# Kernel optimization log

Hardware: AMD Instinct MI355X
Metric: run time of the kernel (lower is better)

The kernel has to match this reference:

```python
import jax, jax.numpy as jnp
import numpy as np

N = 50000; E = 600000; D = 128; NB = 20; L = 3; H = 64; NG = 512; ZMAX = 100
CUTOFF = 5.0

def setup_inputs() -> dict:
    key = jax.random.key(0)
    ks = jax.random.split(key, 32)
    inp = {}
    inp['at_no'] = jax.random.randint(ks[0], (N,), 0, ZMAX)
    inp['pos'] = jax.random.normal(ks[1], (N, 3), dtype=jnp.float32) * 3.0
    inp['edge_index'] = jax.random.randint(ks[2], (2, E), 0, N)
    inp['batch'] = jnp.sort(jax.random.randint(ks[3], (N,), 0, NG))
    def w(k, shape, fan_in):
        return (jax.random.normal(k, shape, dtype=jnp.float32) / np.sqrt(fan_in)).astype(jnp.float32)
    inp['emb'] = w(ks[4], (ZMAX, D), 1.0)
    # per-block filter net: rbf -> 3D
    inp['Wf'] = w(ks[5], (L, NB, 3 * D), NB); inp['bf'] = jnp.zeros((L, 3 * D), jnp.float32)
    # per-block message scalar MLP: D -> D -> 3D
    inp['Wm1'] = w(ks[6], (L, D, D), D);      inp['bm1'] = jnp.zeros((L, D), jnp.float32)
    inp['Wm2'] = w(ks[7], (L, D, 3 * D), D);  inp['bm2'] = jnp.zeros((L, 3 * D), jnp.float32)
    # per-block update: U, V channel-mixing on vectors; MLP 2D -> D -> 3D
    inp['U'] = w(ks[8], (L, D, D), D)
    inp['V'] = w(ks[9], (L, D, D), D)
    inp['Wu1'] = w(ks[10], (L, 2 * D, D), 2 * D); inp['bu1'] = jnp.zeros((L, D), jnp.float32)
    inp['Wu2'] = w(ks[11], (L, D, 3 * D), D);     inp['bu2'] = jnp.zeros((L, 3 * D), jnp.float32)
    # scalar output head: D -> H -> 1, graph sum
    inp['Wo1'] = w(ks[12], (D, H), D); inp['bo1'] = jnp.zeros((H,), jnp.float32)
    inp['Wo2'] = w(ks[13], (H, 1), H); inp['bo2'] = jnp.zeros((1,), jnp.float32)
    return inp

def _painn(at_no, pos, edge_index, batch, emb, Wf, bf, Wm1, bm1, Wm2, bm2,
           U, V, Wu1, bu1, Wu2, bu2, Wo1, bo1, Wo2, bo2):
    src, dst = edge_index[0], edge_index[1]
    vec = pos[dst] - pos[src]                       # [E,3]
    dist = jnp.sqrt(jnp.sum(vec * vec, axis=-1, keepdims=True) + 1e-12)  # [E,1]
    dirv = vec / dist                               # [E,3] (rsh l=1)
    n = jnp.arange(1, NB + 1, dtype=jnp.float32)
    rbf = jnp.sin(n * jnp.pi * dist / CUTOFF) / dist            # [E,NB] Bessel
    fcut = 0.5 * (jnp.cos(jnp.pi * dist / CUTOFF) + 1.0) * (dist < CUTOFF)  # [E,1]

    x = emb[at_no]                                  # [N,D]
    v = jnp.zeros((x.shape[0], 3, D), x.dtype)      # [N,3,D]

    for l in range(L):
        # ---- message ----
        filt = (rbf @ Wf[l] + bf[l]) * fcut                     # [E,3D]
        phi = jax.nn.silu(x @ Wm1[l] + bm1[l]) @ Wm2[l] + bm2[l]  # [N,3D]
        m = phi[src] * filt                                     # [E,3D]
        ds, dv1, dv2 = m[:, :D], m[:, D:2 * D], m[:, 2 * D:]
        dv = dv1[:, None, :] * dirv[:, :, None] + dv2[:, None, :] * v[src]  # [E,3,D]
        x = x + jax.ops.segment_sum(ds, dst, num_segments=N)
        v = v + jax.ops.segment_sum(dv, dst, num_segments=N)
        # ---- update ----
        Uv = jnp.einsum('ncd,de->nce', v, U[l])
        Vv = jnp.einsum('ncd,de->nce', v, V[l])
        Vn = jnp.sqrt(jnp.sum(Vv * Vv, axis=1) + 1e-8)          # [N,D]
        a = jax.nn.silu(jnp.concatenate([x, Vn], axis=-1) @ Wu1[l] + bu1[l]) @ Wu2[l] + bu2[l]
        avv, asv, ass = a[:, :D], a[:, D:2 * D], a[:, 2 * D:]
        x = x + ass + asv * jnp.sum(Uv * Vv, axis=1)
        v = v + avv[:, None, :] * Uv

    node_out = jax.nn.silu(x @ Wo1 + bo1) @ Wo2 + bo2           # [N,1]
    return jax.ops.segment_sum(node_out, batch, num_segments=NG)  # [NG,1]

def reference(at_no, pos, edge_index, batch, emb, Wf, bf, Wm1, bm1, Wm2, bm2,
              U, V, Wu1, bu1, Wu2, bu2, Wo1, bo1, Wo2, bo2):
    return _painn(at_no, pos, edge_index, batch, emb, Wf, bf, Wm1, bm1, Wm2, bm2,
                  U, V, Wu1, bu1, Wu2, bu2, Wo1, bo1, Wo2, bo2)
```

## Files before the change

### kernel.cpp

```cpp
#include <hip/hip_runtime.h>
#include <math.h>

#define NN 50000
#define NE 600000
#define ECAP 230000
#define DD 128
#define D3 384
#define NB_ 20
#define HH 64
#define NG_ 512
#define LSZ 180224

typedef short v8s __attribute__((ext_vector_type(8)));
typedef short v4sh __attribute__((ext_vector_type(4)));
typedef float v4f __attribute__((ext_vector_type(4)));

__device__ __forceinline__ float silu_f(float z) { return z / (1.0f + expf(-z)); }

__device__ __forceinline__ short f2bf(float f) {
  unsigned u = __float_as_uint(f);
  u += 0x7FFF + ((u >> 16) & 1);
  return (short)(u >> 16);
}
__device__ __forceinline__ float bf2f(short s) {
  return __uint_as_float(((unsigned)(unsigned short)s) << 16);
}
__device__ __forceinline__ void split2(float x, short& h, short& l) {
  h = f2bf(x);
  l = f2bf(x - bf2f(h));
}
#define SPLIT8(f0, f1, ah, al) { short h,l; \
  split2(f0.x,h,l); ah[0]=h; al[0]=l;  split2(f0.y,h,l); ah[1]=h; al[1]=l; \
  split2(f0.z,h,l); ah[2]=h; al[2]=l;  split2(f0.w,h,l); ah[3]=h; al[3]=l; \
  split2(f1.x,h,l); ah[4]=h; al[4]=l;  split2(f1.y,h,l); ah[5]=h; al[5]=l; \
  split2(f1.z,h,l); ah[6]=h; al[6]=l;  split2(f1.w,h,l); ah[7]=h; al[7]=l; }
__device__ __forceinline__ void split_store4(float4 f, short* hp, short* lp) {
  short h0,l0,h1,l1,h2,l2,h3,l3;
  split2(f.x,h0,l0); split2(f.y,h1,l1); split2(f.z,h2,l2); split2(f.w,h3,l3);
  v4sh hv = {h0,h1,h2,h3}, lv = {l0,l1,l2,l3};
  *(v4sh*)hp = hv; *(v4sh*)lp = lv;
}
#define MFMA3(acc, ah, al, bh, bl) \
  acc = __builtin_amdgcn_mfma_f32_16x16x32_bf16(ah, bh, acc, 0, 0, 0); \
  acc = __builtin_amdgcn_mfma_f32_16x16x32_bf16(al, bh, acc, 0, 0, 0); \
  acc = __builtin_amdgcn_mfma_f32_16x16x32_bf16(ah, bl, acc, 0, 0, 0);

__global__ void zero_f_kernel(float* __restrict__ p, long n) {
  long i = (long)blockIdx.x * blockDim.x + threadIdx.x;
  long s = (long)gridDim.x * blockDim.x;
  for (; i < n; i += s) p[i] = 0.0f;
}

__global__ void zero_i_kernel(int* __restrict__ p, long n) {
  long i = (long)blockIdx.x * blockDim.x + threadIdx.x;
  long s = (long)gridDim.x * blockDim.x;
  for (; i < n; i += s) p[i] = 0;
}

__global__ void init_x_kernel(const int* __restrict__ at_no, const float* __restrict__ emb,
                              float* __restrict__ x) {
  int i = blockIdx.x * blockDim.x + threadIdx.x;
  if (i >= NN * DD) return;
  x[i] = emb[at_no[i >> 7] * DD + (i & 127)];
}

__global__ void prep_w_kernel(const float* __restrict__ Wm1, const float* __restrict__ Wm2,
                              const float* __restrict__ U, const float* __restrict__ V,
                              const float* __restrict__ Wu1, const float* __restrict__ Wu2,
                              short* __restrict__ hi, short* __restrict__ lo) {
  int idx = blockIdx.x * 256 + threadIdx.x;
  if (idx >= 3 * LSZ) return;
  int l = idx / LSZ, r = idx % LSZ;
  const float* src; int K, N, nk;
  if (r < 16384)       { src = Wm1 + (size_t)l*16384; K = 128; N = 128; nk = r; }
  else if (r < 65536)  { src = Wm2 + (size_t)l*49152; K = 128; N = 384; nk = r - 16384; }
  else if (r < 81920)  { src = U   + (size_t)l*16384; K = 128; N = 128; nk = r - 65536; }
  else if (r < 98304)  { src = V   + (size_t)l*16384; K = 128; N = 128; nk = r - 81920; }
  else if (r < 131072) { src = Wu1 + (size_t)l*32768; K = 256; N = 128; nk = r - 98304; }
  else                 { src = Wu2 + (size_t)l*49152; K = 128; N = 384; nk = r - 131072; }
  int n = nk / K, k = nk - n * K;
  float xx = src[(size_t)k * N + n];
  short h = f2bf(xx);
  hi[idx] = h;
  lo[idx] = f2bf(xx - bf2f(h));
}

__global__ void hist_kernel(const int* __restrict__ ei, const float* __restrict__ pos,
                            int* __restrict__ counts) {
  int e = blockIdx.x * blockDim.x + threadIdx.x;
  if (e >= NE) return;
  int s = ei[e], d = ei[NE + e];
  float dx = pos[3*d]   - pos[3*s];
  float dy = pos[3*d+1] - pos[3*s+1];
  float dz = pos[3*d+2] - pos[3*s+2];
  float d2 = dx*dx + dy*dy + dz*dz + 1e-12f;
  if (d2 < 25.0f) atomicAdd(&counts[d], 1);
}

__global__ void scan_kernel(const int* __restrict__ counts, int* __restrict__ indptr, int n) {
  __shared__ int sm[1024];
  __shared__ int carry_s;
  if (threadIdx.x == 0) carry_s = 0;
  __syncthreads();
  for (int start = 0; start < n; start += 1024) {
    int i = start + (int)threadIdx.x;
    int val = (i < n) ? counts[i] : 0;
    sm[threadIdx.x] = val;
    __syncthreads();
    for (int off = 1; off < 1024; off <<= 1) {
      int t = (threadIdx.x >= (unsigned)off) ? sm[threadIdx.x - off] : 0;
      __syncthreads();
      sm[threadIdx.x] += t;
      __syncthreads();
    }
    int c = carry_s;
    if (i < n) indptr[i] = c + sm[threadIdx.x] - val;
    __syncthreads();
    if (threadIdx.x == 0) carry_s = c + sm[1023];
    __syncthreads();
  }
  if (threadIdx.x == 0) indptr[n] = carry_s;
}

__global__ void fill_kernel(const int* __restrict__ ei, const float* __restrict__ pos,
                            const int* __restrict__ indptr, int* __restrict__ cursor,
                            int* __restrict__ srcs, float4* __restrict__ eg1,
                            float4* __restrict__ eg2) {
  int e = blockIdx.x * blockDim.x + threadIdx.x;
  if (e >= NE) return;
  int s = ei[e], d = ei[NE + e];
  float dx = pos[3*d]   - pos[3*s];
  float dy = pos[3*d+1] - pos[3*s+1];
  float dz = pos[3*d+2] - pos[3*s+2];
  float d2 = dx*dx + dy*dy + dz*dz + 1e-12f;
  if (d2 < 25.0f) {
    int p = atomicAdd(&cursor[d], 1);
    int slot = indptr[d] + p;
    float dist = sqrtf(d2);
    float inv = 1.0f / dist;
    float wang = 0.62831853071795864769f * dist;
    float s1 = __sinf(wang), c1 = __cosf(wang);
    float fc = 0.5f * (c1 + 1.0f);
    srcs[slot] = s;
    eg1[slot] = make_float4(s1, c1, fc, fc * inv);
    eg2[slot] = make_float4(dx * inv, dy * inv, dz * inv, 0.0f);
  }
}

__global__ void __launch_bounds__(512) mlp_phi_kernel(
    const float* __restrict__ x,
    const short* __restrict__ W1h, const short* __restrict__ W1l, const float* __restrict__ b1,
    const short* __restrict__ W2h, const short* __restrict__ W2l, const float* __restrict__ b2,
    float* __restrict__ C0, float* __restrict__ C1, float* __restrict__ C2, int M) {
  __shared__ short sm[4 * 32 * 136];
  #define XH_(r,c) sm[(r)*136 + (c)]
  #define XL_(r,c) sm[4352 + (r)*136 + (c)]
  #define TH_(r,c) sm[8704 + (r)*136 + (c)]
  #define TL_(r,c) sm[13056 + (r)*136 + (c)]
  int tid = threadIdx.x;
  long r0 = (long)blockIdx.x * 32;
  #pragma unroll
  for (int i = 0; i < 2; i++) {
    int lin = i*512 + tid;
    int r = lin >> 5, c4 = lin & 31;
    long row = r0 + r; if (row >= M) row = M - 1;
    float4 f = *(const float4*)(x + row*128 + c4*4);
    split_store4(f, &XH_(r, c4*4), &XL_(r, c4*4));
  }
  __syncthreads();
  int lane = tid & 63, wv = tid >> 6;
  int l15 = lane & 15, q = lane >> 4;
  {
    int n = wv*16 + l15;
    v4f acc[2] = {};
    #pragma unroll
    for (int s = 0; s < 4; s++) {
      v8s bh = *(const v8s*)(W1h + (long)n*128 + s*32 + q*8);
      v8s bl = *(const v8s*)(W1l + (long)n*128 + s*32 + q*8);
      #pragma unroll
      for (int mt = 0; mt < 2; mt++) {
        v8s ah = *(const v8s*)&XH_(mt*16 + l15, s*32 + q*8);
        v8s al = *(const v8s*)&XL_(mt*16 + l15, s*32 + q*8);
        MFMA3(acc[mt], ah, al, bh, bl);
      }
    }
    float bb = b1[n];
    #pragma unroll
    for (int mt = 0; mt < 2; mt++)
      #pragma unroll
      for (int i = 0; i < 4; i++) {
        short h, l;
        split2(silu_f(acc[mt][i] + bb), h, l);
        TH_(mt*16 + q*4 + i, n) = h;
        TL_(mt*16 + q*4 + i, n) = l;
      }
  }
  __syncthreads();
  v4f acc[2][3] = {};
  #pragma unroll
  for (int s = 0; s < 4; s++) {
    v8s ah[2], al[2];
    #pragma unroll
    for (int mt = 0; mt < 2; mt++) {
      ah[mt] = *(const v8s*)&TH_(mt*16 + l15, s*32 + q*8);
      al[mt] = *(const v8s*)&TL_(mt*16 + l15, s*32 + q*8);
    }
    #pragma unroll
    for (int j = 0; j < 3; j++) {
      int n = (wv*3 + j)*16 + l15;
      v8s bh = *(const v8s*)(W2h + (long)n*128 + s*32 + q*8);
      v8s bl = *(const v8s*)(W2l + (long)n*128 + s*32 + q*8);
      #pragma unroll
      for (int mt = 0; mt < 2; mt++) { MFMA3(acc[mt][j], ah[mt], al[mt], bh, bl); }
    }
  }
  #pragma unroll
  for (int j = 0; j < 3; j++) {
    int n = (wv*3 + j)*16 + l15;
    int sl = n >> 7, col = n & 127;
    float* C = (sl == 0) ? C0 : (sl == 1) ? C1 : C2;
    float bb = b2[n];
    #pragma unroll
    for (int mt = 0; mt < 2; mt++)
      #pragma unroll
      for (int i = 0; i < 4; i++) {
        long row = r0 + mt*16 + q*4 + i;
        if (row < M) C[row*128 + col] = acc[mt][j][i] + bb;
      }
  }
  #undef XH_
  #undef XL_
  #undef TH_
  #undef TL_
}

__global__ void __launch_bounds__(512) muva_kernel(
    const float* __restrict__ phi0, const float* __restrict__ phi1,
    const float* __restrict__ phi2, const float* __restrict__ vA,
    float* __restrict__ vB, float* __restrict__ x,
    const int* __restrict__ srcs, const float4* __restrict__ eg1,
    const float4* __restrict__ eg2, const int* __restrict__ indptr,
    const float* __restrict__ Wf_l, const float* __restrict__ bf_l,
    const short* __restrict__ Uth, const short* __restrict__ Utl,
    const short* __restrict__ Vth, const short* __restrict__ Vtl,
    const short* __restrict__ W1h, const short* __restrict__ W1l, const float* __restrict__ b1,
    const short* __restrict__ W2h, const short* __restrict__ W2l, const float* __restrict__ b2) {
  __shared__ float smem[8896];
  short* sms = (short*)smem;
  #define VN(r,c)   smem[(r)*140 + (c)]
  #define XN(r,c)   smem[6720 + (r)*136 + (c)]
  #define VNH(r,c)  sms[(r)*136 + (c)]
  #define VNL(r,c)  sms[6528 + (r)*136 + (c)]
  #define CATH(r,c) sms[(r)*264 + (c)]
  #define CATL(r,c) sms[4224 + (r)*264 + (c)]
  #define T2H(r,c)  sms[8448 + (r)*136 + (c)]
  #define T2L(r,c)  sms[10624 + (r)*136 + (c)]
  const long NND = (long)NN*DD;
  int tid = threadIdx.x;
  long nb = (long)blockIdx.x * 16;
  {
    int g = tid >> 7, d = tid & 127;
    float wf0[NB_], wf1[NB_], wf2[NB_];
    #pragma unroll
    for (int k = 0; k < NB_; k++) {
      wf0[k] = Wf_l[k*D3 + d];
      wf1[k] = Wf_l[k*D3 + DD + d];
      wf2[k] = Wf_l[k*D3 + 2*DD + d];
    }
    float bf0 = bf_l[d], bf1 = bf_l[DD + d], bf2 = bf_l[2*DD + d];
    for (int j = 0; j < 4; j++) {
      int nr = 4*g + j;
      long n = nb + nr;
      int t = indptr[n], end = indptr[n+1];
      float xacc = 0.f, a0 = 0.f, a1 = 0.f, a2 = 0.f;
      float4 g1C = {}, g2C = {};
      float p0C = 0.f, p1C = 0.f, p2C = 0.f, w0C = 0.f, w1C = 0.f, w2C = 0.f;
      if (t < end) {
        int s0 = srcs[t]; g1C = eg1[t]; g2C = eg2[t];
        long b = (long)s0*DD + d;
        p0C = phi0[b]; p1C = phi1[b]; p2C = phi2[b];
        w0C = vA[b]; w1C = vA[NND + b]; w2C = vA[2*NND + b];
      }
      for (; t < end; t++) {
        float4 gg = g1C, dv = g2C;
        float p0 = p0C, p1 = p1C, p2 = p2C, w0 = w0C, w1 = w1C, w2 = w2C;
        if (t + 1 < end) {
          int sN = srcs[t+1]; g1C = eg1[t+1]; g2C = eg2[t+1];
          long b = (long)sN*DD + d;
          p0C = phi0[b]; p1C = phi1[b]; p2C = phi2[b];
          w0C = vA[b]; w1C = vA[NND + b]; w2C = vA[2*NND + b];
        }
        float c2 = 2.0f * gg.y;
        float rkm1 = 0.f, rk = gg.x, dot0 = 0.f, dot1 = 0.f, dot2 = 0.f;
        #pragma unroll
        for (int k = 0; k < NB_; k++) {
          dot0 = fmaf(rk, wf0[k], dot0);
          dot1 = fmaf(rk, wf1[k], dot1);
          dot2 = fmaf(rk, wf2[k], dot2);
          float rn = fmaf(c2, rk, -rkm1);
          rkm1 = rk; rk = rn;
        }
        xacc = fmaf(p0, bf0*gg.z + gg.w*dot0, xacc);
        float m1 = p1 * (bf1*gg.z + gg.w*dot1);
        float m2 = p2 * (bf2*gg.z + gg.w*dot2);
        a0 = fmaf(m1, dv.x, fmaf(m2, w0, a0));
        a1 = fmaf(m1, dv.y, fmaf(m2, w1, a1));
        a2 = fmaf(m1, dv.z, fmaf(m2, w2, a2));
      }
      long b = n*DD + d;
      XN(nr, d) = x[b] + xacc;
      VN(nr, d)      = vA[b]         + a0;
      VN(16 + nr, d) = vA[NND + b]   + a1;
      VN(32 + nr, d) = vA[2*NND + b] + a2;
    }
  }
  __syncthreads();
  int lane = tid & 63, wv = tid >> 6;
  int l15 = lane & 15, q = lane >> 4;
  int d = wv*16 + l15;
  float vold[4][3];
  #pragma unroll
  for (int i = 0; i < 4; i++)
    #pragma unroll
    for (int c = 0; c < 3; c++) vold[i][c] = VN(c*16 + q*4 + i, d);
  float4 cf[3];
  {
    int ch = tid * 3;
    #pragma unroll
    for (int j = 0; j < 3; j++) {
      int r = (ch + j) >> 5, c4 = (ch + j) & 31;
      cf[j] = *(const float4*)&VN(r, c4*4);
    }
  }
  __syncthreads();
  {
    int ch = tid * 3;
    #pragma unroll
    for (int j = 0; j < 3; j++) {
      int r = (ch + j) >> 5, c4 = (ch + j) & 31;
      split_store4(cf[j], &VNH(r, c4*4), &VNL(r, c4*4));
    }
  }
  __syncthreads();
  v4f aU[3] = {}, aV[3] = {};
  #pragma unroll
  for (int s = 0; s < 4; s++) {
    long boff = (long)d*128 + s*32 + q*8;
    v8s buh = *(const v8s*)(Uth + boff);
    v8s bul = *(const v8s*)(Utl + boff);
    v8s bvh = *(const v8s*)(Vth + boff);
    v8s bvl = *(const v8s*)(Vtl + boff);
    #pragma unroll
    for (int c = 0; c < 3; c++) {
      v8s ah = *(const v8s*)&VNH(c*16 + l15, s*32 + q*8);
      v8s al = *(const v8s*)&VNL(c*16 + l15, s*32 + q*8);
      MFMA3(aU[c], ah, al, buh, bul);
      MFMA3(aV[c], ah, al, bvh, bvl);
    }
  }
  float sreg[4], vn2[4];
  #pragma unroll
  for (int i = 0; i < 4; i++) {
    sreg[i] = aU[0][i]*aV[0][i] + aU[1][i]*aV[1][i] + aU[2][i]*aV[2][i];
    vn2[i]  = aV[0][i]*aV[0][i] + aV[1][i]*aV[1][i] + aV[2][i]*aV[2][i];
  }
  __syncthreads();
  {
    int r = tid >> 5, c4 = tid & 31;
    float4 f = *(const float4*)&XN(r, c4*4);
    split_store4(f, &CATH(r, c4*4), &CATL(r, c4*4));
  }
  #pragma unroll
  for (int i = 0; i < 4; i++) {
    short h, l;
    split2(sqrtf(vn2[i] + 1e-8f), h, l);
    CATH(q*4 + i, 128 + d) = h;
    CATL(q*4 + i, 128 + d) = l;
  }
  __syncthreads();
  {
    v4f acc = {};
    #pragma unroll
    for (int s = 0; s < 8; s++) {
      v8s ah = *(const v8s*)&CATH(l15, s*32 + q*8);
      v8s al = *(const v8s*)&CATL(l15, s*32 + q*8);
      v8s bh = *(const v8s*)(W1h + (long)d*256 + s*32 + q*8);
      v8s bl = *(const v8s*)(W1l + (long)d*256 + s*32 + q*8);
      MFMA3(acc, ah, al, bh, bl);
    }
    float bb = b1[d];
    #pragma unroll
    for (int i = 0; i < 4; i++) {
      short h, l;
      split2(silu_f(acc[i] + bb), h, l);
      T2H(q*4 + i, d) = h;
      T2L(q*4 + i, d) = l;
    }
  }
  __syncthreads();
  {
    v4f acc[3] = {};
    #pragma unroll
    for (int s = 0; s < 4; s++) {
      v8s ah = *(const v8s*)&T2H(l15, s*32 + q*8);
      v8s al = *(const v8s*)&T2L(l15, s*32 + q*8);
      #pragma unroll
      for (int g = 0; g < 3; g++) {
        int n = g*128 + d;
        v8s bh = *(const v8s*)(W2h + (long)n*128 + s*32 + q*8);
        v8s bl = *(const v8s*)(W2l + (long)n*128 + s*32 + q*8);
        MFMA3(acc[g], ah, al, bh, bl);
      }
    }
    float bavv = b2[d], basv = b2[128 + d], bass = b2[256 + d];
    #pragma unroll
    for (int i = 0; i < 4; i++) {
      int lr = q*4 + i;
      long row = nb + lr;
      float avv = acc[0][i] + bavv;
      float asv = acc[1][i] + basv;
      float ass = acc[2][i] + bass;
      x[row*DD + d] = XN(lr, d) + ass + asv * sreg[i];
      #pragma unroll
      for (int c = 0; c < 3; c++)
        vB[(long)c*NND + row*DD + d] = fmaf(avv, aU[c][i], vold[i][c]);
    }
  }
  #undef VN
  #undef XN
  #undef VNH
  #undef VNL
  #undef CATH
  #undef CATL
  #undef T2H
  #undef T2L
}

__global__ void __launch_bounds__(256) out_kernel(
    const float* __restrict__ x, const float* __restrict__ Wo1,
    const float* __restrict__ bo1, const float* __restrict__ Wo2,
    const float* __restrict__ bo2, const int* __restrict__ batch,
    float* __restrict__ out) {
  __shared__ float xs[4][132];
  int tid = threadIdx.x;
  long n0 = (long)blockIdx.x * 4;
  if (tid < 128) {
    int r = tid >> 5, c4 = tid & 31;
    *(float4*)&xs[r][c4*4] = *(const float4*)(x + (n0 + r)*128 + c4*4);
  }
  __syncthreads();
  int wv = tid >> 6, t = tid & 63;
  float acc = bo1[t];
  #pragma unroll 16
  for (int k = 0; k < DD; k++) acc = fmaf(xs[wv][k], Wo1[k*HH + t], acc);
  float val = silu_f(acc) * Wo2[t];
  #pragma unroll
  for (int off = 32; off > 0; off >>= 1) val += __shfl_down(val, off);
  if (t == 0) atomicAdd(&out[batch[n0 + wv]], val + bo2[0]);
}

extern "C" void kernel_launch(void* const* d_in, const int* in_sizes, int n_in,
                              void* d_out, int out_size, void* d_ws, size_t ws_size,
                              hipStream_t stream) {
  const int*   at_no = (const int*)d_in[0];
  const float* pos   = (const float*)d_in[1];
  const int*   ei    = (const int*)d_in[2];
  const int*   batch = (const int*)d_in[3];
  const float* emb   = (const float*)d_in[4];
  const float* Wf    = (const float*)d_in[5];
  const float* bfp   = (const float*)d_in[6];
  const float* Wm1   = (const float*)d_in[7];
  const float* bm1   = (const float*)d_in[8];
  const float* Wm2   = (const float*)d_in[9];
  const float* bm2   = (const float*)d_in[10];
  const float* U     = (const float*)d_in[11];
  const float* V     = (const float*)d_in[12];
  const float* Wu1   = (const float*)d_in[13];
  const float* bu1   = (const float*)d_in[14];
  const float* Wu2   = (const float*)d_in[15];
  const float* bu2   = (const float*)d_in[16];
  const float* Wo1   = (const float*)d_in[17];
  const float* bo1   = (const float*)d_in[18];
  const float* Wo2   = (const float*)d_in[19];
  const float* bo2   = (const float*)d_in[20];
  float* out = (float*)d_out;

  char* w = (char*)d_ws;
  auto alloc = [&](size_t bytes) -> void* {
    void* p = (void*)w;
    w += (bytes + 255) & ~(size_t)255;
    return p;
  };
  float*  x      = (float*)alloc(sizeof(float)*(size_t)NN*DD);
  float*  v_a    = (float*)alloc(sizeof(float)*(size_t)NN*D3);
  float*  v_b    = (float*)alloc(sizeof(float)*(size_t)NN*D3);
  float*  t1     = (float*)alloc(sizeof(float)*(size_t)NN*DD);
  float*  phiS   = (float*)alloc(sizeof(float)*(size_t)NN*DD);
  float*  phi0   = (float*)alloc(sizeof(float)*(size_t)NN*DD);
  short*  wbh    = (short*)alloc(sizeof(short)*(size_t)3*LSZ);
  short*  wbl    = (short*)alloc(sizeof(short)*(size_t)3*LSZ);
  int*    srcs   = (int*)alloc(sizeof(int)*(size_t)ECAP);
  float4* eg1    = (float4*)alloc(sizeof(float4)*(size_t)ECAP);
  float4* eg2    = (float4*)alloc(sizeof(float4)*(size_t)ECAP);
  int*    indptr = (int*)alloc(sizeof(int)*((size_t)NN+1));
  int*    counts = (int*)alloc(sizeof(int)*(size_t)NN);

  if ((size_t)(w - (char*)d_ws) > ws_size) {
    zero_f_kernel<<<2, 256, 0, stream>>>(out, NG_);
    return;
  }

  zero_f_kernel<<<2048, 256, 0, stream>>>(v_a, (long)NN*D3);
  zero_f_kernel<<<2, 256, 0, stream>>>(out, NG_);
  zero_i_kernel<<<64, 256, 0, stream>>>(counts, NN);
  init_x_kernel<<<(NN*DD + 255)/256, 256, 0, stream>>>(at_no, emb, x);
  prep_w_kernel<<<(3*LSZ + 255)/256, 256, 0, stream>>>(Wm1, Wm2, U, V, Wu1, Wu2, wbh, wbl);
  hist_kernel<<<(NE + 255)/256, 256, 0, stream>>>(ei, pos, counts);
  scan_kernel<<<1, 1024, 0, stream>>>(counts, indptr, NN);
  zero_i_kernel<<<64, 256, 0, stream>>>(counts, NN);
  fill_kernel<<<(NE + 255)/256, 256, 0, stream>>>(ei, pos, indptr, counts, srcs, eg1, eg2);

  const int MB = (NN + 31) / 32;
  float* vcur = v_a;
  float* vnext = v_b;
  for (int l = 0; l < 3; l++) {
    const float* Wf_l  = Wf  + (size_t)l*NB_*D3;
    const float* bf_l  = bfp + (size_t)l*D3;
    const float* bm1_l = bm1 + (size_t)l*DD;
    const float* bm2_l = bm2 + (size_t)l*D3;
    const float* bu1_l = bu1 + (size_t)l*DD;
    const float* bu2_l = bu2 + (size_t)l*D3;
    const short* Lh = wbh + (size_t)l*LSZ;
    const short* Ll = wbl + (size_t)l*LSZ;
    const short* Wm1h = Lh,          *Wm1L = Ll;
    const short* Wm2h = Lh + 16384,  *Wm2L = Ll + 16384;
    const short* Uh   = Lh + 65536,  *UL   = Ll + 65536;
    const short* Vh   = Lh + 81920,  *VL   = Ll + 81920;
    const short* Wu1h = Lh + 98304,  *Wu1L = Ll + 98304;
    const short* Wu2h = Lh + 131072, *Wu2L = Ll + 131072;

    mlp_phi_kernel<<<MB, 512, 0, stream>>>(x, Wm1h, Wm1L, bm1_l, Wm2h, Wm2L, bm2_l,
                                           phi0, phiS, t1, NN);
    muva_kernel<<<NN/16, 512, 0, stream>>>(phi0, phiS, t1, vcur, vnext, x,
                                           srcs, eg1, eg2, indptr, Wf_l, bf_l,
                                           Uh, UL, Vh, VL,
                                           Wu1h, Wu1L, bu1_l, Wu2h, Wu2L, bu2_l);

    float* tmp = vcur; vcur = vnext; vnext = tmp;
  }

  out_kernel<<<NN/4, 256, 0, stream>>>(x, Wo1, bo1, Wo2, bo2, batch, out);

  (void)in_sizes; (void)n_in; (void)out_size; (void)ws_size;
}
```

Measured before the change: 1.438 ms.

## Software-pipeline muva edge gather across node groups with double-buffered prefetch

The per-node edge loop in muva_kernel becomes one continuous loop over all edges of a 4-node group. It double-buffers the neighbor gathers two edges ahead and prefetches source indices four edges ahead, so loads overlap compute without stalling at node boundaries. The residual loads of x and vA are moved out of the gather phase into coalesced float4 reads issued before the barrier, and launch bounds now request higher occupancy. This adds register pressure and more complex control flow, which the occupancy hint may turn into spills.

```diff
diff --git a/kernel.cpp b/kernel.cpp
--- a/kernel.cpp
+++ b/kernel.cpp
@@ -29,11 +29,6 @@
   h = f2bf(x);
   l = f2bf(x - bf2f(h));
 }
-#define SPLIT8(f0, f1, ah, al) { short h,l; \
-  split2(f0.x,h,l); ah[0]=h; al[0]=l;  split2(f0.y,h,l); ah[1]=h; al[1]=l; \
-  split2(f0.z,h,l); ah[2]=h; al[2]=l;  split2(f0.w,h,l); ah[3]=h; al[3]=l; \
-  split2(f1.x,h,l); ah[4]=h; al[4]=l;  split2(f1.y,h,l); ah[5]=h; al[5]=l; \
-  split2(f1.z,h,l); ah[6]=h; al[6]=l;  split2(f1.w,h,l); ah[7]=h; al[7]=l; }
 __device__ __forceinline__ void split_store4(float4 f, short* hp, short* lp) {
   short h0,l0,h1,l1,h2,l2,h3,l3;
   split2(f.x,h0,l0); split2(f.y,h1,l1); split2(f.z,h2,l2); split2(f.w,h3,l3);
@@ -234,7 +229,7 @@
   #undef TL_
 }
 
-__global__ void __launch_bounds__(512) muva_kernel(
+__global__ void __launch_bounds__(512, 4) muva_kernel(
     const float* __restrict__ phi0, const float* __restrict__ phi1,
     const float* __restrict__ phi2, const float* __restrict__ vA,
     float* __restrict__ vB, float* __restrict__ x,
@@ -259,7 +254,8 @@
   int tid = threadIdx.x;
   long nb = (long)blockIdx.x * 16;
   {
-    int g = tid >> 7, d = tid & 127;
+    int gs = __builtin_amdgcn_readfirstlane((int)(tid >> 7));
+    int d  = tid & 127;
     float wf0[NB_], wf1[NB_], wf2[NB_];
     #pragma unroll
     for (int k = 0; k < NB_; k++) {
@@ -268,69 +264,112 @@
       wf2[k] = Wf_l[k*D3 + 2*DD + d];
     }
     float bf0 = bf_l[d], bf1 = bf_l[DD + d], bf2 = bf_l[2*DD + d];
-    for (int j = 0; j < 4; j++) {
-      int nr = 4*g + j;
-      long n = nb + nr;
-      int t = indptr[n], end = indptr[n+1];
-      float xacc = 0.f, a0 = 0.f, a1 = 0.f, a2 = 0.f;
-      float4 g1C = {}, g2C = {};
-      float p0C = 0.f, p1C = 0.f, p2C = 0.f, w0C = 0.f, w1C = 0.f, w2C = 0.f;
-      if (t < end) {
-        int s0 = srcs[t]; g1C = eg1[t]; g2C = eg2[t];
-        long b = (long)s0*DD + d;
-        p0C = phi0[b]; p1C = phi1[b]; p2C = phi2[b];
-        w0C = vA[b]; w1C = vA[NND + b]; w2C = vA[2*NND + b];
-      }
-      for (; t < end; t++) {
-        float4 gg = g1C, dv = g2C;
-        float p0 = p0C, p1 = p1C, p2 = p2C, w0 = w0C, w1 = w1C, w2 = w2C;
-        if (t + 1 < end) {
-          int sN = srcs[t+1]; g1C = eg1[t+1]; g2C = eg2[t+1];
-          long b = (long)sN*DD + d;
-          p0C = phi0[b]; p1C = phi1[b]; p2C = phi2[b];
-          w0C = vA[b]; w1C = vA[NND + b]; w2C = vA[2*NND + b];
-        }
-        float c2 = 2.0f * gg.y;
-        float rkm1 = 0.f, rk = gg.x, dot0 = 0.f, dot1 = 0.f, dot2 = 0.f;
-        #pragma unroll
-        for (int k = 0; k < NB_; k++) {
-          dot0 = fmaf(rk, wf0[k], dot0);
-          dot1 = fmaf(rk, wf1[k], dot1);
-          dot2 = fmaf(rk, wf2[k], dot2);
-          float rn = fmaf(c2, rk, -rkm1);
-          rkm1 = rk; rk = rn;
-        }
-        xacc = fmaf(p0, bf0*gg.z + gg.w*dot0, xacc);
-        float m1 = p1 * (bf1*gg.z + gg.w*dot1);
-        float m2 = p2 * (bf2*gg.z + gg.w*dot2);
-        a0 = fmaf(m1, dv.x, fmaf(m2, w0, a0));
-        a1 = fmaf(m1, dv.y, fmaf(m2, w1, a1));
-        a2 = fmaf(m1, dv.z, fmaf(m2, w2, a2));
-      }
-      long b = n*DD + d;
-      XN(nr, d) = x[b] + xacc;
-      VN(nr, d)      = vA[b]         + a0;
-      VN(16 + nr, d) = vA[NND + b]   + a1;
-      VN(32 + nr, d) = vA[2*NND + b] + a2;
-    }
-  }
-  __syncthreads();
+    long n0g = nb + 4*gs;
+    int b0  = __builtin_amdgcn_readfirstlane(indptr[n0g]);
+    int b1_ = __builtin_amdgcn_readfirstlane(indptr[n0g+1]);
+    int b2_ = __builtin_amdgcn_readfirstlane(indptr[n0g+2]);
+    int b3_ = __builtin_amdgcn_readfirstlane(indptr[n0g+3]);
+    int b4_ = __builtin_amdgcn_readfirstlane(indptr[n0g+4]);
+    int sA = 0, sB = 0;
+    float p0A=0,p1A=0,p2A=0,w0A=0,w1A=0,w2A=0;
+    float p0B=0,p1B=0,p2B=0,w0B=0,w1B=0,w2B=0;
+    float4 g1A={}, g2A={}, g1B={}, g2B={};
+    if (b0 < b4_) {
+      int s0 = srcs[b0];
+      long bb = (long)s0*DD + d;
+      p0A = phi0[bb]; p1A = phi1[bb]; p2A = phi2[bb];
+      w0A = vA[bb]; w1A = vA[NND+bb]; w2A = vA[2*NND+bb];
+      g1A = eg1[b0]; g2A = eg2[b0];
+    }
+    if (b0 + 1 < b4_) {
+      int s1v = srcs[b0+1];
+      long bb = (long)s1v*DD + d;
+      p0B = phi0[bb]; p1B = phi1[bb]; p2B = phi2[bb];
+      w0B = vA[bb]; w1B = vA[NND+bb]; w2B = vA[2*NND+bb];
+      g1B = eg1[b0+1]; g2B = eg2[b0+1];
+    }
+    if (b0 + 2 < b4_) sA = srcs[b0+2];
+    if (b0 + 3 < b4_) sB = srcs[b0+3];
+    float xacc=0.f, a0=0.f, a1=0.f, a2=0.f;
+    int e = b0, cur = 0, nxt = b1_;
+#define SW_BODY(P0,P1,P2,W0,W1,W2, G1, G2, SS) \
+    { while (e >= nxt) { int nr = 4*gs + cur; \
+        XN(nr, d) = xacc; VN(nr, d) = a0; VN(16+nr, d) = a1; VN(32+nr, d) = a2; \
+        xacc = 0.f; a0 = 0.f; a1 = 0.f; a2 = 0.f; \
+        cur++; nxt = (cur == 1) ? b2_ : (cur == 2) ? b3_ : b4_; } \
+      float c2 = 2.0f * G1.y; \
+      float rkm1 = 0.f, rk = G1.x, dot0 = 0.f, dot1 = 0.f, dot2 = 0.f; \
+      _Pragma("unroll") \
+      for (int k = 0; k < NB_; k++) { \
+        dot0 = fmaf(rk, wf0[k], dot0); \
+        dot1 = fmaf(rk, wf1[k], dot1); \
+        dot2 = fmaf(rk, wf2[k], dot2); \
+        float rn = fmaf(c2, rk, -rkm1); \
+        rkm1 = rk; rk = rn; } \
+      xacc = fmaf(P0, bf0*G1.z + G1.w*dot0, xacc); \
+      float m1 = P1 * (bf1*G1.z + G1.w*dot1); \
+      float m2 = P2 * (bf2*G1.z + G1.w*dot2); \
+      a0 = fmaf(m1, G2.x, fmaf(m2, W0, a0)); \
+      a1 = fmaf(m1, G2.y, fmaf(m2, W1, a1)); \
+      a2 = fmaf(m1, G2.z, fmaf(m2, W2, a2)); \
+      if (e + 2 < b4_) { \
+        long bb = (long)SS*DD + d; \
+        P0 = phi0[bb]; P1 = phi1[bb]; P2 = phi2[bb]; \
+        W0 = vA[bb]; W1 = vA[NND+bb]; W2 = vA[2*NND+bb]; \
+        G1 = eg1[e+2]; G2 = eg2[e+2]; } \
+      if (e + 4 < b4_) SS = srcs[e+4]; \
+      ++e; }
+    while (e < b4_) {
+      SW_BODY(p0A,p1A,p2A,w0A,w1A,w2A, g1A, g2A, sA)
+      if (e >= b4_) break;
+      SW_BODY(p0B,p1B,p2B,w0B,w1B,w2B, g1B, g2B, sB)
+    }
+#undef SW_BODY
+    while (cur < 4) {
+      int nr = 4*gs + cur;
+      XN(nr, d) = xacc; VN(nr, d) = a0; VN(16+nr, d) = a1; VN(32+nr, d) = a2;
+      xacc = 0.f; a0 = 0.f; a1 = 0.f; a2 = 0.f;
+      cur++;
+    }
+  }
   int lane = tid & 63, wv = tid >> 6;
   int l15 = lane & 15, q = lane >> 4;
-  int d = wv*16 + l15;
-  float vold[4][3];
-  #pragma unroll
-  for (int i = 0; i < 4; i++)
-    #pragma unroll
-    for (int c = 0; c < 3; c++) vold[i][c] = VN(c*16 + q*4 + i, d);
-  float4 cf[3];
+  int dc = wv*16 + l15;
+  float4 vb4[3]; float4 xb4;
   {
     int ch = tid * 3;
     #pragma unroll
     for (int j = 0; j < 3; j++) {
       int r = (ch + j) >> 5, c4 = (ch + j) & 31;
-      cf[j] = *(const float4*)&VN(r, c4*4);
-    }
+      vb4[j] = *(const float4*)(vA + (long)(r >> 4)*NND + (nb + (r & 15))*DD + c4*4);
+    }
+    int r = tid >> 5, c4 = tid & 31;
+    xb4 = *(const float4*)(x + (nb + r)*DD + c4*4);
+  }
+  float vbold[4][3];
+  #pragma unroll
+  for (int i = 0; i < 4; i++)
+    #pragma unroll
+    for (int c = 0; c < 3; c++)
+      vbold[i][c] = vA[(long)c*NND + (nb + q*4 + i)*DD + dc];
+  __syncthreads();
+  float voldd[4][3];
+  #pragma unroll
+  for (int i = 0; i < 4; i++)
+    #pragma unroll
+    for (int c = 0; c < 3; c++) voldd[i][c] = VN(c*16 + q*4 + i, dc);
+  float4 cf[3];
+  {
+    int ch = tid * 3;
+    #pragma unroll
+    for (int j = 0; j < 3; j++) {
+      int r = (ch + j) >> 5, c4 = (ch + j) & 31;
+      float4 t = *(const float4*)&VN(r, c4*4);
+      cf[j] = make_float4(vb4[j].x + t.x, vb4[j].y + t.y, vb4[j].z + t.z, vb4[j].w + t.w);
+    }
+    int r = tid >> 5, c4 = tid & 31;
+    float4 t = *(float4*)&XN(r, c4*4);
+    *(float4*)&XN(r, c4*4) = make_float4(xb4.x + t.x, xb4.y + t.y, xb4.z + t.z, xb4.w + t.w);
   }
   __syncthreads();
   {
@@ -345,7 +384,7 @@
   v4f aU[3] = {}, aV[3] = {};
   #pragma unroll
   for (int s = 0; s < 4; s++) {
-    long boff = (long)d*128 + s*32 + q*8;
+    long boff = (long)dc*128 + s*32 + q*8;
     v8s buh = *(const v8s*)(Uth + boff);
     v8s bul = *(const v8s*)(Utl + boff);
     v8s bvh = *(const v8s*)(Vth + boff);
@@ -374,8 +413,8 @@
   for (int i = 0; i < 4; i++) {
     short h, l;
     split2(sqrtf(vn2[i] + 1e-8f), h, l);
-    CATH(q*4 + i, 128 + d) = h;
-    CATL(q*4 + i, 128 + d) = l;
+    CATH(q*4 + i, 128 + dc) = h;
+    CATL(q*4 + i, 128 + dc) = l;
   }
   __syncthreads();
   {
@@ -384,17 +423,17 @@
     for (int s = 0; s < 8; s++) {
       v8s ah = *(const v8s*)&CATH(l15, s*32 + q*8);
       v8s al = *(const v8s*)&CATL(l15, s*32 + q*8);
-      v8s bh = *(const v8s*)(W1h + (long)d*256 + s*32 + q*8);
-      v8s bl = *(const v8s*)(W1l + (long)d*256 + s*32 + q*8);
+      v8s bh = *(const v8s*)(W1h + (long)dc*256 + s*32 + q*8);
+      v8s bl = *(const v8s*)(W1l + (long)dc*256 + s*32 + q*8);
       MFMA3(acc, ah, al, bh, bl);
     }
-    float bb = b1[d];
+    float bb = b1[dc];
     #pragma unroll
     for (int i = 0; i < 4; i++) {
       short h, l;
       split2(silu_f(acc[i] + bb), h, l);
-      T2H(q*4 + i, d) = h;
-      T2L(q*4 + i, d) = l;
+      T2H(q*4 + i, dc) = h;
+      T2L(q*4 + i, dc) = l;
     }
   }
   __syncthreads();
@@ -406,13 +445,13 @@
       v8s al = *(const v8s*)&T2L(l15, s*32 + q*8);
       #pragma unroll
       for (int g = 0; g < 3; g++) {
-        int n = g*128 + d;
+        int n = g*128 + dc;
         v8s bh = *(const v8s*)(W2h + (long)n*128 + s*32 + q*8);
         v8s bl = *(const v8s*)(W2l + (long)n*128 + s*32 + q*8);
         MFMA3(acc[g], ah, al, bh, bl);
       }
     }
-    float bavv = b2[d], basv = b2[128 + d], bass = b2[256 + d];
+    float bavv = b2[dc], basv = b2[128 + dc], bass = b2[256 + dc];
     #pragma unroll
     for (int i = 0; i < 4; i++) {
       int lr = q*4 + i;
@@ -420,10 +459,10 @@
       float avv = acc[0][i] + bavv;
       float asv = acc[1][i] + basv;
       float ass = acc[2][i] + bass;
-      x[row*DD + d] = XN(lr, d) + ass + asv * sreg[i];
+      x[row*DD + dc] = XN(lr, dc) + ass + asv * sreg[i];
       #pragma unroll
       for (int c = 0; c < 3; c++)
-        vB[(long)c*NND + row*DD + d] = fmaf(avv, aU[c][i], vold[i][c]);
+        vB[(long)c*NND + row*DD + dc] = fmaf(avv, aU[c][i], voldd[i][c] + vbold[i][c]);
     }
   }
   #undef VN
```

Result: faster. 1.360 ms (-5.4%).
